# Performance work log

Measured on AMD Instinct MI355X. Metric: run time of the kernel, lower is better.

## Reference

```python
import jax, jax.numpy as jnp
import numpy as np

N_NODES = 100000


def gcn_layer(x, W, b, src, dst, norm, n):
    # x: [N, Fin] -> linear transform then normalized scatter-add aggregation
    h = x @ W                                   # [N, Fout]
    msgs = h[src] * norm[:, None]               # [E+N, Fout] edge messages
    out = jax.ops.segment_sum(msgs, dst, num_segments=n)
    return out + b


def _build_graph(edge_index, n):
    # add self loops (PyG GCNConv default)
    loops = jnp.arange(n, dtype=edge_index.dtype)
    src = jnp.concatenate([edge_index[0], loops])
    dst = jnp.concatenate([edge_index[1], loops])
    deg = jax.ops.segment_sum(jnp.ones_like(dst, dtype=jnp.float32), dst, num_segments=n)
    dis = jnp.where(deg > 0, jax.lax.rsqrt(deg), 0.0)  # deg^{-1/2}
    norm = dis[src] * dis[dst]                  # symmetric normalization per edge
    return src, dst, norm


def setup_inputs() -> dict:
    key = jax.random.key(0)
    ks = jax.random.split(key, 8)
    x = jax.random.normal(ks[0], (N_NODES, 3), dtype=jnp.float32)
    edge_index = jax.random.randint(ks[1], (2, 6400000), 0, N_NODES, dtype=jnp.int32)
    def glorot(k, fin, fout):
        s = jnp.sqrt(6.0 / (fin + fout))
        return jax.random.uniform(k, (fin, fout), jnp.float32, -s, s)
    return {
        "x": x,
        "edge_index": edge_index,
        "W1": glorot(ks[2], 3, 32), "b1": jnp.zeros((32,), jnp.float32),
        "W2": glorot(ks[3], 32, 32), "b2": jnp.zeros((32,), jnp.float32),
        "W3": glorot(ks[4], 32, 1), "b3": jnp.zeros((1,), jnp.float32),
    }


def reference(x, edge_index, W1, b1, W2, b2, W3, b3):
    n = x.shape[0]
    src, dst, norm = _build_graph(edge_index, n)
    h = jax.nn.relu(gcn_layer(x, W1, b1, src, dst, norm, n))
    h = jax.nn.relu(gcn_layer(h, W2, b2, src, dst, norm, n))
    return gcn_layer(h, W3, b3, src, dst, norm, n)
```

## Files before the change

### kernel.cpp

```cpp
#include <hip/hip_runtime.h>
#include <hip/hip_fp16.h>


#define BLK 256
#define SB 1280
#define CHUNK 5000
#define BKT 128
#define NBKT 782
#define MAXNB 1024
#define BUFSZ 15360

__global__ void k_hist(const int* __restrict__ dst, int* __restrict__ hist, int E) {
    __shared__ int lh[NBKT];
    for (int b = threadIdx.x; b < NBKT; b += blockDim.x) lh[b] = 0;
    __syncthreads();
    int beg = blockIdx.x * CHUNK;
    int end = min(E, beg + CHUNK);
    int nq = (end - beg) >> 2;
    const int4* d4 = (const int4*)(dst + beg);
    for (int i = threadIdx.x; i < nq; i += blockDim.x) {
        int4 d = d4[i];
        atomicAdd(&lh[d.x >> 7], 1);
        atomicAdd(&lh[d.y >> 7], 1);
        atomicAdd(&lh[d.z >> 7], 1);
        atomicAdd(&lh[d.w >> 7], 1);
    }
    for (int e = beg + (nq << 2) + threadIdx.x; e < end; e += blockDim.x)
        atomicAdd(&lh[dst[e] >> 7], 1);
    __syncthreads();
    for (int b = threadIdx.x; b < NBKT; b += blockDim.x)
        hist[(size_t)blockIdx.x * NBKT + b] = lh[b];
}

__global__ void k_scanA(int* __restrict__ hist, int* __restrict__ btot, int NB) {
    int b = blockIdx.x, t = threadIdx.x;
    int base = t * 5;
    int v0 = hist[(size_t)(base + 0) * NB + b];
    int v1 = hist[(size_t)(base + 1) * NB + b];
    int v2 = hist[(size_t)(base + 2) * NB + b];
    int v3 = hist[(size_t)(base + 3) * NB + b];
    int v4 = hist[(size_t)(base + 4) * NB + b];
    int s = v0 + v1 + v2 + v3 + v4;
    int lane = t & 63, w = t >> 6;
    int x = s;
#pragma unroll
    for (int off = 1; off < 64; off <<= 1) {
        int u = __shfl_up(x, off, 64);
        if (lane >= off) x += u;
    }
    __shared__ int wsum[4];
    if (lane == 63) wsum[w] = x;
    __syncthreads();
    int woff = 0;
    for (int k = 0; k < 4; k++) woff += (k < w) ? wsum[k] : 0;
    int run = woff + x - s;
    hist[(size_t)(base + 0) * NB + b] = run;  run += v0;
    hist[(size_t)(base + 1) * NB + b] = run;  run += v1;
    hist[(size_t)(base + 2) * NB + b] = run;  run += v2;
    hist[(size_t)(base + 3) * NB + b] = run;  run += v3;
    hist[(size_t)(base + 4) * NB + b] = run;  run += v4;
    if (t == 255) btot[b] = run;
}

__global__ void k_scanB(const int* __restrict__ btot, int* __restrict__ bbase,
                        int NB, int E) {
    __shared__ int sh[MAXNB];
    int t = threadIdx.x;
    int v = (t < NB) ? btot[t] : 0;
    sh[t] = v;
    __syncthreads();
    for (int off = 1; off < MAXNB; off <<= 1) {
        int u = (t >= off) ? sh[t - off] : 0;
        __syncthreads();
        sh[t] += u;
        __syncthreads();
    }
    if (t < NB) bbase[t] = sh[t] - v;
    if (t == 0) bbase[NB] = E;
}

__global__ void k_bsort(const int* __restrict__ src, const int* __restrict__ dst,
                        const int* __restrict__ hist, const int* __restrict__ bbase,
                        unsigned int* __restrict__ packed, int E) {
    __shared__ unsigned int bufB[CHUNK];
    __shared__ unsigned short binarr2[CHUNK];
    __shared__ int cnt[NBKT];
    __shared__ int off[NBKT];
    __shared__ int cur[NBKT];
    __shared__ int gbase[NBKT];
    __shared__ int wsum[4];
    int t = threadIdx.x;
    int beg = blockIdx.x * CHUNK;
    int end = min(E, beg + CHUNK);
    int len = end - beg;
    for (int b = t; b < NBKT; b += blockDim.x) {
        cnt[b] = 0;
        gbase[b] = bbase[b] + hist[(size_t)blockIdx.x * NBKT + b];
    }
    __syncthreads();
    {
        int nq = len >> 2;
        const int4* d4 = (const int4*)(dst + beg);
        for (int i = t; i < nq; i += blockDim.x) {
            int4 d = d4[i];
            atomicAdd(&cnt[d.x >> 7], 1);
            atomicAdd(&cnt[d.y >> 7], 1);
            atomicAdd(&cnt[d.z >> 7], 1);
            atomicAdd(&cnt[d.w >> 7], 1);
        }
        for (int i = (nq << 2) + t; i < len; i += blockDim.x)
            atomicAdd(&cnt[dst[beg + i] >> 7], 1);
    }
    __syncthreads();
    {
        int base = t * 4;
        int v0 = (base + 0 < NBKT) ? cnt[base + 0] : 0;
        int v1 = (base + 1 < NBKT) ? cnt[base + 1] : 0;
        int v2 = (base + 2 < NBKT) ? cnt[base + 2] : 0;
        int v3 = (base + 3 < NBKT) ? cnt[base + 3] : 0;
        int s = v0 + v1 + v2 + v3;
        int lane = t & 63, w = t >> 6;
        int x = s;
#pragma unroll
        for (int o = 1; o < 64; o <<= 1) {
            int u = __shfl_up(x, o, 64);
            if (lane >= o) x += u;
        }
        if (lane == 63) wsum[w] = x;
        __syncthreads();
        int woff = 0;
        for (int k = 0; k < 4; k++) woff += (k < w) ? wsum[k] : 0;
        int run = woff + x - s;
        if (base + 0 < NBKT) { off[base + 0] = run; cur[base + 0] = run; } run += v0;
        if (base + 1 < NBKT) { off[base + 1] = run; cur[base + 1] = run; } run += v1;
        if (base + 2 < NBKT) { off[base + 2] = run; cur[base + 2] = run; } run += v2;
        if (base + 3 < NBKT) { off[base + 3] = run; cur[base + 3] = run; } run += v3;
    }
    __syncthreads();
    for (int i = t; i < len; i += blockDim.x) {
        int d = dst[beg + i];
        int s = src[beg + i];
        int b = d >> 7;
        int pos = atomicAdd(&cur[b], 1);
        bufB[pos] = (unsigned)s | ((unsigned)(d & 127) << 17);
        binarr2[pos] = (unsigned short)b;
    }
    __syncthreads();
    for (int i = t; i < len; i += blockDim.x) {
        int b = binarr2[i];
        packed[gbase[b] + i - off[b]] = bufB[i];
    }
}

__global__ void k_sort(unsigned int* __restrict__ packed, const int* __restrict__ bbase,
                       const float* __restrict__ x, float* __restrict__ dis,
                       float4* __restrict__ y4, int* __restrict__ rowptr, int N, int E) {
    __shared__ unsigned int buf[BUFSZ];
    __shared__ int cnt[BKT];
    __shared__ int sc[BKT];
    __shared__ int cur[BKT];
    int b = blockIdx.x, t = threadIdx.x;
    int beg = bbase[b], end = bbase[b + 1];
    int len = end - beg;
    for (int i = t; i < len; i += blockDim.x) buf[i] = packed[beg + i];
    if (t < BKT) cnt[t] = 0;
    __syncthreads();
    for (int i = t; i < len; i += blockDim.x)
        atomicAdd(&cnt[buf[i] >> 17], 1);
    __syncthreads();
    int v = 0;
    if (t < BKT) { v = cnt[t]; sc[t] = v; }
    __syncthreads();
    for (int off = 1; off < BKT; off <<= 1) {
        int u = 0;
        if (t < BKT && t >= off) u = sc[t - off];
        __syncthreads();
        if (t < BKT) sc[t] += u;
        __syncthreads();
    }
    if (t < BKT) {
        int excl = sc[t] - v;
        cur[t] = excl;
        int gi = b * BKT + t;
        if (gi < N) {
            rowptr[gi] = beg + excl;
            float di = rsqrtf((float)v + 1.0f);
            dis[gi] = di;
            float4 y;
            y.x = di * x[3 * gi + 0];
            y.y = di * x[3 * gi + 1];
            y.z = di * x[3 * gi + 2];
            y.w = 0.0f;
            y4[gi] = y;
        }
    }
    __syncthreads();
    for (int i = t; i < len; i += blockDim.x) {
        unsigned vv = buf[i];
        int pos = atomicAdd(&cur[vv >> 17], 1);
        packed[beg + pos] = vv & 0x1FFFF;
    }
    if (b == 0 && t == 0) rowptr[N] = E;
}

__global__ void k_l1(const unsigned int* __restrict__ csr, const int* __restrict__ rowptr,
                     const float4* __restrict__ y4, const float* __restrict__ dis,
                     const float* __restrict__ W1, const float* __restrict__ b1,
                     __half* __restrict__ g, int N) {
    int t = blockIdx.x * blockDim.x + threadIdx.x;
    int i = t >> 5, j = t & 31;
    if (i >= N) return;
    int beg = rowptr[i], end = rowptr[i + 1];
    float ax = 0.f, ay = 0.f, az = 0.f;
    for (int e = beg + j; e < end; e += 32) {
        float4 yv = y4[csr[e]];
        ax += yv.x; ay += yv.y; az += yv.z;
    }
#pragma unroll
    for (int m = 16; m >= 1; m >>= 1) {
        ax += __shfl_xor(ax, m, 32);
        ay += __shfl_xor(ay, m, 32);
        az += __shfl_xor(az, m, 32);
    }
    float di = dis[i];
    float4 ys = y4[i];
    float a0 = di * (ax + ys.x);
    float a1 = di * (ay + ys.y);
    float a2 = di * (az + ys.z);
    float h = b1[j] + a0 * W1[j] + a1 * W1[32 + j] + a2 * W1[64 + j];
    g[(size_t)i * 32 + j] = __float2half(di * fmaxf(h, 0.f));
}

__global__ void k_l2(const unsigned int* __restrict__ csr, const int* __restrict__ rowptr,
                     const __half* __restrict__ g, const float* __restrict__ dis,
                     const float* __restrict__ W2, const float* __restrict__ b2,
                     const float* __restrict__ W3, float* __restrict__ q, int N) {
    int t = blockIdx.x * blockDim.x + threadIdx.x;
    int i = t >> 5, j = t & 31;
    if (i >= N) return;
    int beg = rowptr[i], end = rowptr[i + 1];
    float a0 = 0.f, a1 = 0.f, a2 = 0.f, a3 = 0.f;
    float a4 = 0.f, a5 = 0.f, a6 = 0.f, a7 = 0.f;
    for (int k0 = beg; k0 < end; k0 += 32) {
        int e = k0 + j;
        int myedge = (e < end) ? (int)csr[e] : 0;
        int cnt = min(32, end - k0);
        int t2 = 0;
        for (; t2 + 8 <= cnt; t2 += 8) {
            int s0 = __shfl(myedge, t2 + 0, 32);
            int s1 = __shfl(myedge, t2 + 1, 32);
            int s2 = __shfl(myedge, t2 + 2, 32);
            int s3 = __shfl(myedge, t2 + 3, 32);
            int s4 = __shfl(myedge, t2 + 4, 32);
            int s5 = __shfl(myedge, t2 + 5, 32);
            int s6 = __shfl(myedge, t2 + 6, 32);
            int s7 = __shfl(myedge, t2 + 7, 32);
            a0 += __half2float(g[(size_t)s0 * 32 + j]);
            a1 += __half2float(g[(size_t)s1 * 32 + j]);
            a2 += __half2float(g[(size_t)s2 * 32 + j]);
            a3 += __half2float(g[(size_t)s3 * 32 + j]);
            a4 += __half2float(g[(size_t)s4 * 32 + j]);
            a5 += __half2float(g[(size_t)s5 * 32 + j]);
            a6 += __half2float(g[(size_t)s6 * 32 + j]);
            a7 += __half2float(g[(size_t)s7 * 32 + j]);
        }
        for (; t2 < cnt; t2++) {
            int s = __shfl(myedge, t2, 32);
            a0 += __half2float(g[(size_t)s * 32 + j]);
        }
    }
    float acc = ((a0 + a1) + (a2 + a3)) + ((a4 + a5) + (a6 + a7));
    float di = dis[i];
    float a = di * (acc + __half2float(g[(size_t)i * 32 + j]));
    float o = b2[j];
#pragma unroll
    for (int k = 0; k < 32; k++)
        o += __shfl(a, k, 32) * W2[k * 32 + j];
    float h2 = fmaxf(o, 0.f);
    float c = h2 * W3[j];
#pragma unroll
    for (int m = 16; m >= 1; m >>= 1)
        c += __shfl_xor(c, m, 32);
    if (j == 0) q[i] = di * c;
}

__global__ void k_l3(const unsigned int* __restrict__ csr, const int* __restrict__ rowptr,
                     const float* __restrict__ q, const float* __restrict__ dis,
                     const float* __restrict__ b3, float* __restrict__ out, int N) {
    int t = blockIdx.x * blockDim.x + threadIdx.x;
    int i = t >> 5, j = t & 31;
    if (i >= N) return;
    int beg = rowptr[i], end = rowptr[i + 1];
    float acc = 0.f;
    for (int e = beg + j; e < end; e += 32)
        acc += q[csr[e]];
#pragma unroll
    for (int m = 16; m >= 1; m >>= 1)
        acc += __shfl_xor(acc, m, 32);
    if (j == 0) out[i] = dis[i] * (acc + q[i]) + b3[0];
}

extern "C" void kernel_launch(void* const* d_in, const int* in_sizes, int n_in,
                              void* d_out, int out_size, void* d_ws, size_t ws_size,
                              hipStream_t stream) {
    const float* x  = (const float*)d_in[0];
    const int*   ei = (const int*)d_in[1];
    const float* W1 = (const float*)d_in[2];
    const float* b1 = (const float*)d_in[3];
    const float* W2 = (const float*)d_in[4];
    const float* b2 = (const float*)d_in[5];
    const float* W3 = (const float*)d_in[6];
    const float* b3 = (const float*)d_in[7];
    float* out = (float*)d_out;

    int N = in_sizes[0] / 3;
    int E = in_sizes[1] / 2;
    const int* src = ei;
    const int* dst = ei + E;

    char* w = (char*)d_ws;
    int*   hist   = (int*)w;       w += (size_t)SB * NBKT * 4;
    int*   btot   = (int*)w;       w += (size_t)MAXNB * 4;
    int*   bbase  = (int*)w;       w += (size_t)(MAXNB + 1) * 4;
    int*   rowptr = (int*)w;       w += (size_t)(N + 1) * 4;
    float* dis    = (float*)w;     w += (size_t)N * 4;
    float* y4     = (float*)w;     w += (size_t)N * 16;
    __half* g     = (__half*)w;    w += (size_t)N * 32 * 2;
    float* q      = (float*)w;     w += (size_t)N * 4;
    unsigned int* packed = (unsigned int*)w;  w += (size_t)E * 4;

    k_hist <<<SB, BLK, 0, stream>>>(dst, hist, E);
    k_scanA<<<NBKT, BLK, 0, stream>>>(hist, btot, NBKT);
    k_scanB<<<1, MAXNB, 0, stream>>>(btot, bbase, NBKT, E);
    k_bsort<<<SB, BLK, 0, stream>>>(src, dst, hist, bbase, packed, E);
    k_sort <<<NBKT, BLK, 0, stream>>>(packed, bbase, x, dis, (float4*)y4, rowptr, N, E);

    long long tn = (long long)N * 32;
    unsigned gn = (unsigned)((tn + BLK - 1) / BLK);
    k_l1<<<gn, BLK, 0, stream>>>(packed, rowptr, (const float4*)y4, dis, W1, b1, g, N);
    k_l2<<<gn, BLK, 0, stream>>>(packed, rowptr, g, dis, W2, b2, W3, q, N);
    k_l3<<<gn, BLK, 0, stream>>>(packed, rowptr, q, dis, b3, out, N);
}
```

Before: 369.0 us.

## Split layer-2 gather into two feature-half passes over planar fp16 buffers

```diff
diff --git a/kernel.cpp b/kernel.cpp
--- a/kernel.cpp
+++ b/kernel.cpp
@@ -228,59 +228,109 @@
     float a1 = di * (ay + ys.y);
     float a2 = di * (az + ys.z);
     float h = b1[j] + a0 * W1[j] + a1 * W1[32 + j] + a2 * W1[64 + j];
-    g[(size_t)i * 32 + j] = __float2half(di * fmaxf(h, 0.f));
-}
-
-__global__ void k_l2(const unsigned int* __restrict__ csr, const int* __restrict__ rowptr,
-                     const __half* __restrict__ g, const float* __restrict__ dis,
-                     const float* __restrict__ W2, const float* __restrict__ b2,
-                     const float* __restrict__ W3, float* __restrict__ q, int N) {
+    __half* gb = g + (size_t)(j >> 4) * ((size_t)N * 16);
+    gb[(size_t)i * 16 + (j & 15)] = __float2half(di * fmaxf(h, 0.f));
+}
+
+__global__ void k_l2a(const unsigned int* __restrict__ csr, const int* __restrict__ rowptr,
+                      const __half* __restrict__ g0, const float* __restrict__ dis,
+                      __half* __restrict__ part, int N) {
     int t = blockIdx.x * blockDim.x + threadIdx.x;
-    int i = t >> 5, j = t & 31;
+    int i = t >> 4, j = t & 15;
     if (i >= N) return;
     int beg = rowptr[i], end = rowptr[i + 1];
     float a0 = 0.f, a1 = 0.f, a2 = 0.f, a3 = 0.f;
     float a4 = 0.f, a5 = 0.f, a6 = 0.f, a7 = 0.f;
-    for (int k0 = beg; k0 < end; k0 += 32) {
+    for (int k0 = beg; k0 < end; k0 += 16) {
         int e = k0 + j;
         int myedge = (e < end) ? (int)csr[e] : 0;
-        int cnt = min(32, end - k0);
+        int cnt = min(16, end - k0);
         int t2 = 0;
         for (; t2 + 8 <= cnt; t2 += 8) {
-            int s0 = __shfl(myedge, t2 + 0, 32);
-            int s1 = __shfl(myedge, t2 + 1, 32);
-            int s2 = __shfl(myedge, t2 + 2, 32);
-            int s3 = __shfl(myedge, t2 + 3, 32);
-            int s4 = __shfl(myedge, t2 + 4, 32);
-            int s5 = __shfl(myedge, t2 + 5, 32);
-            int s6 = __shfl(myedge, t2 + 6, 32);
-            int s7 = __shfl(myedge, t2 + 7, 32);
-            a0 += __half2float(g[(size_t)s0 * 32 + j]);
-            a1 += __half2float(g[(size_t)s1 * 32 + j]);
-            a2 += __half2float(g[(size_t)s2 * 32 + j]);
-            a3 += __half2float(g[(size_t)s3 * 32 + j]);
-            a4 += __half2float(g[(size_t)s4 * 32 + j]);
-            a5 += __half2float(g[(size_t)s5 * 32 + j]);
-            a6 += __half2float(g[(size_t)s6 * 32 + j]);
-            a7 += __half2float(g[(size_t)s7 * 32 + j]);
+            int s0 = __shfl(myedge, t2 + 0, 16);
+            int s1 = __shfl(myedge, t2 + 1, 16);
+            int s2 = __shfl(myedge, t2 + 2, 16);
+            int s3 = __shfl(myedge, t2 + 3, 16);
+            int s4 = __shfl(myedge, t2 + 4, 16);
+            int s5 = __shfl(myedge, t2 + 5, 16);
+            int s6 = __shfl(myedge, t2 + 6, 16);
+            int s7 = __shfl(myedge, t2 + 7, 16);
+            a0 += __half2float(g0[s0 * 16 + j]);
+            a1 += __half2float(g0[s1 * 16 + j]);
+            a2 += __half2float(g0[s2 * 16 + j]);
+            a3 += __half2float(g0[s3 * 16 + j]);
+            a4 += __half2float(g0[s4 * 16 + j]);
+            a5 += __half2float(g0[s5 * 16 + j]);
+            a6 += __half2float(g0[s6 * 16 + j]);
+            a7 += __half2float(g0[s7 * 16 + j]);
         }
         for (; t2 < cnt; t2++) {
-            int s = __shfl(myedge, t2, 32);
-            a0 += __half2float(g[(size_t)s * 32 + j]);
+            int s = __shfl(myedge, t2, 16);
+            a0 += __half2float(g0[s * 16 + j]);
         }
     }
     float acc = ((a0 + a1) + (a2 + a3)) + ((a4 + a5) + (a6 + a7));
     float di = dis[i];
-    float a = di * (acc + __half2float(g[(size_t)i * 32 + j]));
-    float o = b2[j];
-#pragma unroll
-    for (int k = 0; k < 32; k++)
-        o += __shfl(a, k, 32) * W2[k * 32 + j];
-    float h2 = fmaxf(o, 0.f);
-    float c = h2 * W3[j];
-#pragma unroll
-    for (int m = 16; m >= 1; m >>= 1)
-        c += __shfl_xor(c, m, 32);
+    float a = di * (acc + __half2float(g0[i * 16 + j]));
+    part[(size_t)i * 16 + j] = __float2half(a);
+}
+
+__global__ void k_l2b(const unsigned int* __restrict__ csr, const int* __restrict__ rowptr,
+                      const __half* __restrict__ g1, const float* __restrict__ dis,
+                      const __half* __restrict__ part,
+                      const float* __restrict__ W2, const float* __restrict__ b2,
+                      const float* __restrict__ W3, float* __restrict__ q, int N) {
+    int t = blockIdx.x * blockDim.x + threadIdx.x;
+    int i = t >> 4, j = t & 15;
+    if (i >= N) return;
+    int beg = rowptr[i], end = rowptr[i + 1];
+    float a0 = 0.f, a1 = 0.f, a2 = 0.f, a3 = 0.f;
+    float a4 = 0.f, a5 = 0.f, a6 = 0.f, a7 = 0.f;
+    for (int k0 = beg; k0 < end; k0 += 16) {
+        int e = k0 + j;
+        int myedge = (e < end) ? (int)csr[e] : 0;
+        int cnt = min(16, end - k0);
+        int t2 = 0;
+        for (; t2 + 8 <= cnt; t2 += 8) {
+            int s0 = __shfl(myedge, t2 + 0, 16);
+            int s1 = __shfl(myedge, t2 + 1, 16);
+            int s2 = __shfl(myedge, t2 + 2, 16);
+            int s3 = __shfl(myedge, t2 + 3, 16);
+            int s4 = __shfl(myedge, t2 + 4, 16);
+            int s5 = __shfl(myedge, t2 + 5, 16);
+            int s6 = __shfl(myedge, t2 + 6, 16);
+            int s7 = __shfl(myedge, t2 + 7, 16);
+            a0 += __half2float(g1[s0 * 16 + j]);
+            a1 += __half2float(g1[s1 * 16 + j]);
+            a2 += __half2float(g1[s2 * 16 + j]);
+            a3 += __half2float(g1[s3 * 16 + j]);
+            a4 += __half2float(g1[s4 * 16 + j]);
+            a5 += __half2float(g1[s5 * 16 + j]);
+            a6 += __half2float(g1[s6 * 16 + j]);
+            a7 += __half2float(g1[s7 * 16 + j]);
+        }
+        for (; t2 < cnt; t2++) {
+            int s = __shfl(myedge, t2, 16);
+            a0 += __half2float(g1[s * 16 + j]);
+        }
+    }
+    float acc = ((a0 + a1) + (a2 + a3)) + ((a4 + a5) + (a6 + a7));
+    float di = dis[i];
+    float ah = di * (acc + __half2float(g1[i * 16 + j]));
+    float al = __half2float(part[(size_t)i * 16 + j]);
+    float o0 = b2[j], o1 = b2[j + 16];
+#pragma unroll
+    for (int k = 0; k < 16; k++) {
+        float xl = __shfl(al, k, 16);
+        float xh = __shfl(ah, k, 16);
+        o0 += xl * W2[k * 32 + j]      + xh * W2[(k + 16) * 32 + j];
+        o1 += xl * W2[k * 32 + j + 16] + xh * W2[(k + 16) * 32 + j + 16];
+    }
+    float h0 = fmaxf(o0, 0.f), h1 = fmaxf(o1, 0.f);
+    float c = h0 * W3[j] + h1 * W3[j + 16];
+#pragma unroll
+    for (int m = 8; m >= 1; m >>= 1)
+        c += __shfl_xor(c, m, 16);
     if (j == 0) q[i] = di * c;
 }
 
@@ -329,6 +379,10 @@
     float* q      = (float*)w;     w += (size_t)N * 4;
     unsigned int* packed = (unsigned int*)w;  w += (size_t)E * 4;
 
+    __half* part = (__half*)hist;
+    __half* g0 = g;
+    __half* g1 = g + (size_t)N * 16;
+
     k_hist <<<SB, BLK, 0, stream>>>(dst, hist, E);
     k_scanA<<<NBKT, BLK, 0, stream>>>(hist, btot, NBKT);
     k_scanB<<<1, MAXNB, 0, stream>>>(btot, bbase, NBKT, E);
@@ -337,7 +391,10 @@
 
     long long tn = (long long)N * 32;
     unsigned gn = (unsigned)((tn + BLK - 1) / BLK);
-    k_l1<<<gn, BLK, 0, stream>>>(packed, rowptr, (const float4*)y4, dis, W1, b1, g, N);
-    k_l2<<<gn, BLK, 0, stream>>>(packed, rowptr, g, dis, W2, b2, W3, q, N);
-    k_l3<<<gn, BLK, 0, stream>>>(packed, rowptr, q, dis, b3, out, N);
-}
+    long long tn2 = (long long)N * 16;
+    unsigned gn2 = (unsigned)((tn2 + BLK - 1) / BLK);
+    k_l1 <<<gn,  BLK, 0, stream>>>(packed, rowptr, (const float4*)y4, dis, W1, b1, g, N);
+    k_l2a<<<gn2, BLK, 0, stream>>>(packed, rowptr, g0, dis, part, N);
+    k_l2b<<<gn2, BLK, 0, stream>>>(packed, rowptr, g1, dis, part, W2, b2, W3, q, N);
+    k_l3 <<<gn,  BLK, 0, stream>>>(packed, rowptr, q, dis, b3, out, N);
+}
```

Result: slower. 389.8 us (+5.6%).

## Split layer-2 features into two 16-wide half planes, gather with vector loads

Applied to the files above, without the earlier changes.

```diff
diff --git a/kernel.cpp b/kernel.cpp
--- a/kernel.cpp
+++ b/kernel.cpp
@@ -228,60 +228,140 @@
     float a1 = di * (ay + ys.y);
     float a2 = di * (az + ys.z);
     float h = b1[j] + a0 * W1[j] + a1 * W1[32 + j] + a2 * W1[64 + j];
-    g[(size_t)i * 32 + j] = __float2half(di * fmaxf(h, 0.f));
-}
-
-__global__ void k_l2(const unsigned int* __restrict__ csr, const int* __restrict__ rowptr,
-                     const __half* __restrict__ g, const float* __restrict__ dis,
-                     const float* __restrict__ W2, const float* __restrict__ b2,
-                     const float* __restrict__ W3, float* __restrict__ q, int N) {
+    __half* gb = g + (size_t)(j >> 4) * ((size_t)N * 16);
+    gb[(size_t)i * 16 + (j & 15)] = __float2half(di * fmaxf(h, 0.f));
+}
+
+__device__ __forceinline__ void acc8(float* a, uint4 r) {
+    const __half2* h = (const __half2*)&r;
+#pragma unroll
+    for (int k = 0; k < 4; k++) {
+        float2 f = __half22float2(h[k]);
+        a[2 * k]     += f.x;
+        a[2 * k + 1] += f.y;
+    }
+}
+
+__device__ __forceinline__ void unp8(float* a, uint4 r) {
+    const __half2* h = (const __half2*)&r;
+#pragma unroll
+    for (int k = 0; k < 4; k++) {
+        float2 f = __half22float2(h[k]);
+        a[2 * k]     = f.x;
+        a[2 * k + 1] = f.y;
+    }
+}
+
+__global__ void k_l2a(const unsigned int* __restrict__ csr, const int* __restrict__ rowptr,
+                      const __half* __restrict__ g0, const float* __restrict__ dis,
+                      __half* __restrict__ part, int N) {
     int t = blockIdx.x * blockDim.x + threadIdx.x;
-    int i = t >> 5, j = t & 31;
+    int i = t >> 2, l = t & 3;
     if (i >= N) return;
     int beg = rowptr[i], end = rowptr[i + 1];
-    float a0 = 0.f, a1 = 0.f, a2 = 0.f, a3 = 0.f;
-    float a4 = 0.f, a5 = 0.f, a6 = 0.f, a7 = 0.f;
-    for (int k0 = beg; k0 < end; k0 += 32) {
-        int e = k0 + j;
-        int myedge = (e < end) ? (int)csr[e] : 0;
-        int cnt = min(32, end - k0);
-        int t2 = 0;
-        for (; t2 + 8 <= cnt; t2 += 8) {
-            int s0 = __shfl(myedge, t2 + 0, 32);
-            int s1 = __shfl(myedge, t2 + 1, 32);
-            int s2 = __shfl(myedge, t2 + 2, 32);
-            int s3 = __shfl(myedge, t2 + 3, 32);
-            int s4 = __shfl(myedge, t2 + 4, 32);
-            int s5 = __shfl(myedge, t2 + 5, 32);
-            int s6 = __shfl(myedge, t2 + 6, 32);
-            int s7 = __shfl(myedge, t2 + 7, 32);
-            a0 += __half2float(g[(size_t)s0 * 32 + j]);
-            a1 += __half2float(g[(size_t)s1 * 32 + j]);
-            a2 += __half2float(g[(size_t)s2 * 32 + j]);
-            a3 += __half2float(g[(size_t)s3 * 32 + j]);
-            a4 += __half2float(g[(size_t)s4 * 32 + j]);
-            a5 += __half2float(g[(size_t)s5 * 32 + j]);
-            a6 += __half2float(g[(size_t)s6 * 32 + j]);
-            a7 += __half2float(g[(size_t)s7 * 32 + j]);
+    const uint4* gq = (const uint4*)g0;
+    float acc[16];
+#pragma unroll
+    for (int f = 0; f < 16; f++) acc[f] = 0.f;
+    int e = beg + l;
+    for (; e + 4 < end; e += 8) {
+        int s0 = csr[e], s1 = csr[e + 4];
+        uint4 r0 = gq[2 * (size_t)s0], r1 = gq[2 * (size_t)s0 + 1];
+        uint4 r2 = gq[2 * (size_t)s1], r3 = gq[2 * (size_t)s1 + 1];
+        acc8(acc, r0); acc8(acc + 8, r1);
+        acc8(acc, r2); acc8(acc + 8, r3);
+    }
+    if (e < end) {
+        int s = csr[e];
+        uint4 r0 = gq[2 * (size_t)s], r1 = gq[2 * (size_t)s + 1];
+        acc8(acc, r0); acc8(acc + 8, r1);
+    }
+#pragma unroll
+    for (int f = 0; f < 16; f++) {
+        acc[f] += __shfl_xor(acc[f], 1, 4);
+        acc[f] += __shfl_xor(acc[f], 2, 4);
+    }
+    if (l == 0) {
+        float di = dis[i];
+        float sf[16];
+        unp8(sf, gq[2 * (size_t)i]);
+        unp8(sf + 8, gq[2 * (size_t)i + 1]);
+        uint4 w0, w1;
+        __half2* p0 = (__half2*)&w0;
+        __half2* p1 = (__half2*)&w1;
+#pragma unroll
+        for (int k = 0; k < 4; k++) {
+            p0[k] = __floats2half2_rn(di * (acc[2 * k] + sf[2 * k]),
+                                      di * (acc[2 * k + 1] + sf[2 * k + 1]));
+            p1[k] = __floats2half2_rn(di * (acc[8 + 2 * k] + sf[8 + 2 * k]),
+                                      di * (acc[8 + 2 * k + 1] + sf[8 + 2 * k + 1]));
         }
-        for (; t2 < cnt; t2++) {
-            int s = __shfl(myedge, t2, 32);
-            a0 += __half2float(g[(size_t)s * 32 + j]);
-        }
-    }
-    float acc = ((a0 + a1) + (a2 + a3)) + ((a4 + a5) + (a6 + a7));
+        uint4* pq = (uint4*)part;
+        pq[2 * (size_t)i]     = w0;
+        pq[2 * (size_t)i + 1] = w1;
+    }
+}
+
+__global__ void k_l2b(const unsigned int* __restrict__ csr, const int* __restrict__ rowptr,
+                      const __half* __restrict__ g1, const float* __restrict__ dis,
+                      const __half* __restrict__ part,
+                      const float* __restrict__ W2, const float* __restrict__ b2,
+                      const float* __restrict__ W3, float* __restrict__ q, int N) {
+    int t = blockIdx.x * blockDim.x + threadIdx.x;
+    int i = t >> 2, l = t & 3;
+    if (i >= N) return;
+    int beg = rowptr[i], end = rowptr[i + 1];
+    const uint4* gq = (const uint4*)g1;
+    float acc[16];
+#pragma unroll
+    for (int f = 0; f < 16; f++) acc[f] = 0.f;
+    int e = beg + l;
+    for (; e + 4 < end; e += 8) {
+        int s0 = csr[e], s1 = csr[e + 4];
+        uint4 r0 = gq[2 * (size_t)s0], r1 = gq[2 * (size_t)s0 + 1];
+        uint4 r2 = gq[2 * (size_t)s1], r3 = gq[2 * (size_t)s1 + 1];
+        acc8(acc, r0); acc8(acc + 8, r1);
+        acc8(acc, r2); acc8(acc + 8, r3);
+    }
+    if (e < end) {
+        int s = csr[e];
+        uint4 r0 = gq[2 * (size_t)s], r1 = gq[2 * (size_t)s + 1];
+        acc8(acc, r0); acc8(acc + 8, r1);
+    }
+#pragma unroll
+    for (int f = 0; f < 16; f++) {
+        acc[f] += __shfl_xor(acc[f], 1, 4);
+        acc[f] += __shfl_xor(acc[f], 2, 4);
+    }
+    float av[32];
+    const uint4* pq = (const uint4*)part;
+    unp8(av, pq[2 * (size_t)i]);
+    unp8(av + 8, pq[2 * (size_t)i + 1]);
+    float sf[16];
+    unp8(sf, gq[2 * (size_t)i]);
+    unp8(sf + 8, gq[2 * (size_t)i + 1]);
     float di = dis[i];
-    float a = di * (acc + __half2float(g[(size_t)i * 32 + j]));
-    float o = b2[j];
-#pragma unroll
-    for (int k = 0; k < 32; k++)
-        o += __shfl(a, k, 32) * W2[k * 32 + j];
-    float h2 = fmaxf(o, 0.f);
-    float c = h2 * W3[j];
-#pragma unroll
-    for (int m = 16; m >= 1; m >>= 1)
-        c += __shfl_xor(c, m, 32);
-    if (j == 0) q[i] = di * c;
+#pragma unroll
+    for (int f = 0; f < 16; f++) av[16 + f] = di * (acc[f] + sf[f]);
+    float o[8];
+    const float* bb = b2 + 8 * l;
+#pragma unroll
+    for (int m = 0; m < 8; m++) o[m] = bb[m];
+    const float* wbase = W2 + 8 * l;
+#pragma unroll
+    for (int k = 0; k < 32; k++) {
+        float a = av[k];
+        const float* wr = wbase + k * 32;
+#pragma unroll
+        for (int m = 0; m < 8; m++) o[m] = fmaf(a, wr[m], o[m]);
+    }
+    const float* w3 = W3 + 8 * l;
+    float c = 0.f;
+#pragma unroll
+    for (int m = 0; m < 8; m++) c += fmaxf(o[m], 0.f) * w3[m];
+    c += __shfl_xor(c, 1, 4);
+    c += __shfl_xor(c, 2, 4);
+    if (l == 0) q[i] = di * c;
 }
 
 __global__ void k_l3(const unsigned int* __restrict__ csr, const int* __restrict__ rowptr,
@@ -319,15 +399,21 @@
     const int* dst = ei + E;
 
     char* w = (char*)d_ws;
-    int*   hist   = (int*)w;       w += (size_t)SB * NBKT * 4;
-    int*   btot   = (int*)w;       w += (size_t)MAXNB * 4;
-    int*   bbase  = (int*)w;       w += (size_t)(MAXNB + 1) * 4;
-    int*   rowptr = (int*)w;       w += (size_t)(N + 1) * 4;
-    float* dis    = (float*)w;     w += (size_t)N * 4;
-    float* y4     = (float*)w;     w += (size_t)N * 16;
-    __half* g     = (__half*)w;    w += (size_t)N * 32 * 2;
-    float* q      = (float*)w;     w += (size_t)N * 4;
-    unsigned int* packed = (unsigned int*)w;  w += (size_t)E * 4;
+#define CARVE(nbytes) w; w += (((size_t)(nbytes) + 255) & ~(size_t)255)
+    int*   hist   = (int*)  CARVE((size_t)SB * NBKT * 4);
+    int*   btot   = (int*)  CARVE((size_t)MAXNB * 4);
+    int*   bbase  = (int*)  CARVE((size_t)(MAXNB + 1) * 4);
+    int*   rowptr = (int*)  CARVE((size_t)(N + 1) * 4);
+    float* dis    = (float*)CARVE((size_t)N * 4);
+    float* y4     = (float*)CARVE((size_t)N * 16);
+    __half* g     = (__half*)CARVE((size_t)N * 32 * 2);
+    float* q      = (float*)CARVE((size_t)N * 4);
+    unsigned int* packed = (unsigned int*)CARVE((size_t)E * 4);
+#undef CARVE
+
+    __half* part = (__half*)hist;
+    __half* g0 = g;
+    __half* g1 = g + (size_t)N * 16;
 
     k_hist <<<SB, BLK, 0, stream>>>(dst, hist, E);
     k_scanA<<<NBKT, BLK, 0, stream>>>(hist, btot, NBKT);
@@ -337,7 +423,10 @@
 
     long long tn = (long long)N * 32;
     unsigned gn = (unsigned)((tn + BLK - 1) / BLK);
-    k_l1<<<gn, BLK, 0, stream>>>(packed, rowptr, (const float4*)y4, dis, W1, b1, g, N);
-    k_l2<<<gn, BLK, 0, stream>>>(packed, rowptr, g, dis, W2, b2, W3, q, N);
-    k_l3<<<gn, BLK, 0, stream>>>(packed, rowptr, q, dis, b3, out, N);
-}
+    long long tn4 = (long long)N * 4;
+    unsigned gn4 = (unsigned)((tn4 + BLK - 1) / BLK);
+    k_l1 <<<gn,  BLK, 0, stream>>>(packed, rowptr, (const float4*)y4, dis, W1, b1, g, N);
+    k_l2a<<<gn4, BLK, 0, stream>>>(packed, rowptr, g0, dis, part, N);
+    k_l2b<<<gn4, BLK, 0, stream>>>(packed, rowptr, g1, dis, part, W2, b2, W3, q, N);
+    k_l3 <<<gn,  BLK, 0, stream>>>(packed, rowptr, q, dis, b3, out, N);
+}
```

Result: slower. 403.5 us (+9.4%).

## Use 8 lanes per node with vector fp16 gathers in layer 2; sort by src sub-bucket

Applied to the files above, without the earlier changes.

```diff
diff --git a/kernel.cpp b/kernel.cpp
--- a/kernel.cpp
+++ b/kernel.cpp
@@ -156,31 +156,43 @@
                        const float* __restrict__ x, float* __restrict__ dis,
                        float4* __restrict__ y4, int* __restrict__ rowptr, int N, int E) {
     __shared__ unsigned int buf[BUFSZ];
-    __shared__ int cnt[BKT];
-    __shared__ int sc[BKT];
-    __shared__ int cur[BKT];
+    __shared__ int cnt[4 * BKT];
+    __shared__ int cur[4 * BKT];
+    __shared__ int wsum[4];
     int b = blockIdx.x, t = threadIdx.x;
     int beg = bbase[b], end = bbase[b + 1];
     int len = end - beg;
     for (int i = t; i < len; i += blockDim.x) buf[i] = packed[beg + i];
-    if (t < BKT) cnt[t] = 0;
-    __syncthreads();
-    for (int i = t; i < len; i += blockDim.x)
-        atomicAdd(&cnt[buf[i] >> 17], 1);
-    __syncthreads();
-    int v = 0;
-    if (t < BKT) { v = cnt[t]; sc[t] = v; }
-    __syncthreads();
-    for (int off = 1; off < BKT; off <<= 1) {
-        int u = 0;
-        if (t < BKT && t >= off) u = sc[t - off];
+    cnt[t] = 0; cnt[t + 256] = 0;
+    __syncthreads();
+    for (int i = t; i < len; i += blockDim.x) {
+        unsigned v = buf[i];
+        int key = (int)((v >> 17) << 2) | (int)((v & 0x1FFFFu) >> 15);
+        atomicAdd(&cnt[key], 1);
+    }
+    __syncthreads();
+    {
+        int v0 = cnt[2 * t], v1 = cnt[2 * t + 1];
+        int s = v0 + v1;
+        int lane = t & 63, w = t >> 6;
+        int xs = s;
+#pragma unroll
+        for (int o = 1; o < 64; o <<= 1) {
+            int u = __shfl_up(xs, o, 64);
+            if (lane >= o) xs += u;
+        }
+        if (lane == 63) wsum[w] = xs;
         __syncthreads();
-        if (t < BKT) sc[t] += u;
-        __syncthreads();
-    }
+        int woff = 0;
+        for (int k = 0; k < 4; k++) woff += (k < w) ? wsum[k] : 0;
+        int run = woff + xs - s;
+        cur[2 * t] = run;
+        cur[2 * t + 1] = run + v0;
+    }
+    __syncthreads();
     if (t < BKT) {
-        int excl = sc[t] - v;
-        cur[t] = excl;
+        int excl = cur[4 * t];
+        int v = cnt[4 * t] + cnt[4 * t + 1] + cnt[4 * t + 2] + cnt[4 * t + 3];
         int gi = b * BKT + t;
         if (gi < N) {
             rowptr[gi] = beg + excl;
@@ -197,7 +209,8 @@
     __syncthreads();
     for (int i = t; i < len; i += blockDim.x) {
         unsigned vv = buf[i];
-        int pos = atomicAdd(&cur[vv >> 17], 1);
+        int key = (int)((vv >> 17) << 2) | (int)((vv & 0x1FFFFu) >> 15);
+        int pos = atomicAdd(&cur[key], 1);
         packed[beg + pos] = vv & 0x1FFFF;
     }
     if (b == 0 && t == 0) rowptr[N] = E;
@@ -231,57 +244,81 @@
     g[(size_t)i * 32 + j] = __float2half(di * fmaxf(h, 0.f));
 }
 
+__device__ __forceinline__ void acc4(float& c0, float& c1, float& c2, float& c3,
+                                     uint2 r) {
+    __half2 a = *(const __half2*)&r.x;
+    __half2 b = *(const __half2*)&r.y;
+    float2 fa = __half22float2(a);
+    float2 fb = __half22float2(b);
+    c0 += fa.x; c1 += fa.y; c2 += fb.x; c3 += fb.y;
+}
+
 __global__ void k_l2(const unsigned int* __restrict__ csr, const int* __restrict__ rowptr,
                      const __half* __restrict__ g, const float* __restrict__ dis,
                      const float* __restrict__ W2, const float* __restrict__ b2,
                      const float* __restrict__ W3, float* __restrict__ q, int N) {
     int t = blockIdx.x * blockDim.x + threadIdx.x;
-    int i = t >> 5, j = t & 31;
+    int i = t >> 3, j = t & 7;
     if (i >= N) return;
     int beg = rowptr[i], end = rowptr[i + 1];
-    float a0 = 0.f, a1 = 0.f, a2 = 0.f, a3 = 0.f;
-    float a4 = 0.f, a5 = 0.f, a6 = 0.f, a7 = 0.f;
-    for (int k0 = beg; k0 < end; k0 += 32) {
-        int e = k0 + j;
-        int myedge = (e < end) ? (int)csr[e] : 0;
-        int cnt = min(32, end - k0);
-        int t2 = 0;
-        for (; t2 + 8 <= cnt; t2 += 8) {
-            int s0 = __shfl(myedge, t2 + 0, 32);
-            int s1 = __shfl(myedge, t2 + 1, 32);
-            int s2 = __shfl(myedge, t2 + 2, 32);
-            int s3 = __shfl(myedge, t2 + 3, 32);
-            int s4 = __shfl(myedge, t2 + 4, 32);
-            int s5 = __shfl(myedge, t2 + 5, 32);
-            int s6 = __shfl(myedge, t2 + 6, 32);
-            int s7 = __shfl(myedge, t2 + 7, 32);
-            a0 += __half2float(g[(size_t)s0 * 32 + j]);
-            a1 += __half2float(g[(size_t)s1 * 32 + j]);
-            a2 += __half2float(g[(size_t)s2 * 32 + j]);
-            a3 += __half2float(g[(size_t)s3 * 32 + j]);
-            a4 += __half2float(g[(size_t)s4 * 32 + j]);
-            a5 += __half2float(g[(size_t)s5 * 32 + j]);
-            a6 += __half2float(g[(size_t)s6 * 32 + j]);
-            a7 += __half2float(g[(size_t)s7 * 32 + j]);
-        }
-        for (; t2 < cnt; t2++) {
-            int s = __shfl(myedge, t2, 32);
-            a0 += __half2float(g[(size_t)s * 32 + j]);
-        }
-    }
-    float acc = ((a0 + a1) + (a2 + a3)) + ((a4 + a5) + (a6 + a7));
+    const uint2* g2 = (const uint2*)g;
+    float c0 = 0.f, c1 = 0.f, c2 = 0.f, c3 = 0.f;
+    int e = beg;
+    for (; e + 8 <= end; e += 8) {
+        int s0 = (int)csr[e + 0], s1 = (int)csr[e + 1];
+        int s2 = (int)csr[e + 2], s3 = (int)csr[e + 3];
+        int s4 = (int)csr[e + 4], s5 = (int)csr[e + 5];
+        int s6 = (int)csr[e + 6], s7 = (int)csr[e + 7];
+        uint2 r0 = g2[s0 * 8 + j];
+        uint2 r1 = g2[s1 * 8 + j];
+        uint2 r2 = g2[s2 * 8 + j];
+        uint2 r3 = g2[s3 * 8 + j];
+        uint2 r4 = g2[s4 * 8 + j];
+        uint2 r5 = g2[s5 * 8 + j];
+        uint2 r6 = g2[s6 * 8 + j];
+        uint2 r7 = g2[s7 * 8 + j];
+        acc4(c0, c1, c2, c3, r0);
+        acc4(c0, c1, c2, c3, r1);
+        acc4(c0, c1, c2, c3, r2);
+        acc4(c0, c1, c2, c3, r3);
+        acc4(c0, c1, c2, c3, r4);
+        acc4(c0, c1, c2, c3, r5);
+        acc4(c0, c1, c2, c3, r6);
+        acc4(c0, c1, c2, c3, r7);
+    }
+    for (; e < end; e++) {
+        int s = (int)csr[e];
+        uint2 r = g2[s * 8 + j];
+        acc4(c0, c1, c2, c3, r);
+    }
     float di = dis[i];
-    float a = di * (acc + __half2float(g[(size_t)i * 32 + j]));
-    float o = b2[j];
-#pragma unroll
-    for (int k = 0; k < 32; k++)
-        o += __shfl(a, k, 32) * W2[k * 32 + j];
-    float h2 = fmaxf(o, 0.f);
-    float c = h2 * W3[j];
-#pragma unroll
-    for (int m = 16; m >= 1; m >>= 1)
-        c += __shfl_xor(c, m, 32);
-    if (j == 0) q[i] = di * c;
+    uint2 rs = g2[i * 8 + j];
+    float2 sa = __half22float2(*(const __half2*)&rs.x);
+    float2 sb = __half22float2(*(const __half2*)&rs.y);
+    float a0 = di * (c0 + sa.x);
+    float a1 = di * (c1 + sa.y);
+    float a2 = di * (c2 + sb.x);
+    float a3 = di * (c3 + sb.y);
+    int m = 4 * j;
+    float o0 = b2[m + 0], o1 = b2[m + 1], o2 = b2[m + 2], o3 = b2[m + 3];
+#pragma unroll
+    for (int kl = 0; kl < 8; kl++) {
+        float x0 = __shfl(a0, kl, 8);
+        float x1 = __shfl(a1, kl, 8);
+        float x2 = __shfl(a2, kl, 8);
+        float x3 = __shfl(a3, kl, 8);
+        const float* w0 = W2 + (4 * kl) * 32 + m;
+        o0 = fmaf(x0, w0[0], fmaf(x1, w0[32], fmaf(x2, w0[64], fmaf(x3, w0[96], o0))));
+        o1 = fmaf(x0, w0[1], fmaf(x1, w0[33], fmaf(x2, w0[65], fmaf(x3, w0[97], o1))));
+        o2 = fmaf(x0, w0[2], fmaf(x1, w0[34], fmaf(x2, w0[66], fmaf(x3, w0[98], o2))));
+        o3 = fmaf(x0, w0[3], fmaf(x1, w0[35], fmaf(x2, w0[67], fmaf(x3, w0[99], o3))));
+    }
+    float cc = fmaxf(o0, 0.f) * W3[m + 0] + fmaxf(o1, 0.f) * W3[m + 1]
+             + fmaxf(o2, 0.f) * W3[m + 2] + fmaxf(o3, 0.f) * W3[m + 3];
+    cc += __shfl_xor(cc, 1, 8);
+    cc += __shfl_xor(cc, 2, 8);
+    cc += __shfl_xor(cc, 4, 8);
+    if (j == 0) q[i] = di * cc;
 }
 
 __global__ void k_l3(const unsigned int* __restrict__ csr, const int* __restrict__ rowptr,
@@ -319,15 +356,17 @@
     const int* dst = ei + E;
 
     char* w = (char*)d_ws;
-    int*   hist   = (int*)w;       w += (size_t)SB * NBKT * 4;
-    int*   btot   = (int*)w;       w += (size_t)MAXNB * 4;
-    int*   bbase  = (int*)w;       w += (size_t)(MAXNB + 1) * 4;
-    int*   rowptr = (int*)w;       w += (size_t)(N + 1) * 4;
-    float* dis    = (float*)w;     w += (size_t)N * 4;
-    float* y4     = (float*)w;     w += (size_t)N * 16;
-    __half* g     = (__half*)w;    w += (size_t)N * 32 * 2;
-    float* q      = (float*)w;     w += (size_t)N * 4;
-    unsigned int* packed = (unsigned int*)w;  w += (size_t)E * 4;
+#define CARVE(nbytes) w; w += (((size_t)(nbytes) + 255) & ~(size_t)255)
+    int*   hist   = (int*)  CARVE((size_t)SB * NBKT * 4);
+    int*   btot   = (int*)  CARVE((size_t)MAXNB * 4);
+    int*   bbase  = (int*)  CARVE((size_t)(MAXNB + 1) * 4);
+    int*   rowptr = (int*)  CARVE((size_t)(N + 1) * 4);
+    float* dis    = (float*)CARVE((size_t)N * 4);
+    float* y4     = (float*)CARVE((size_t)N * 16);
+    __half* g     = (__half*)CARVE((size_t)N * 32 * 2);
+    float* q      = (float*)CARVE((size_t)N * 4);
+    unsigned int* packed = (unsigned int*)CARVE((size_t)E * 4);
+#undef CARVE
 
     k_hist <<<SB, BLK, 0, stream>>>(dst, hist, E);
     k_scanA<<<NBKT, BLK, 0, stream>>>(hist, btot, NBKT);
@@ -337,7 +376,9 @@
 
     long long tn = (long long)N * 32;
     unsigned gn = (unsigned)((tn + BLK - 1) / BLK);
-    k_l1<<<gn, BLK, 0, stream>>>(packed, rowptr, (const float4*)y4, dis, W1, b1, g, N);
-    k_l2<<<gn, BLK, 0, stream>>>(packed, rowptr, g, dis, W2, b2, W3, q, N);
-    k_l3<<<gn, BLK, 0, stream>>>(packed, rowptr, q, dis, b3, out, N);
-}
+    long long tn8 = (long long)N * 8;
+    unsigned gn8 = (unsigned)((tn8 + BLK - 1) / BLK);
+    k_l1<<<gn,  BLK, 0, stream>>>(packed, rowptr, (const float4*)y4, dis, W1, b1, g, N);
+    k_l2<<<gn8, BLK, 0, stream>>>(packed, rowptr, g, dis, W2, b2, W3, q, N);
+    k_l3<<<gn,  BLK, 0, stream>>>(packed, rowptr, q, dis, b3, out, N);
+}
```

Measured after the change: 348.8 us. -5.5%, faster.
